# Optimization experiments

Measured on AMD Instinct MI355X. Metric: run time of the kernel, lower is better.

## Reference

```python
import jax, jax.numpy as jnp
import numpy as np

EPS = 1e-5  # BatchNorm3d default eps


def setup_inputs() -> dict:
    key = jax.random.key(0)
    ks = jax.random.split(key, 8)
    B, C, T, H, W = 2, 256, 8, 28, 28
    P, NS = 128, 5
    sc = 0.02  # keep activations stable through 5 residual stages
    return {
        "x": jax.random.normal(ks[0], (B, C, T, H, W), jnp.float32),
        "Wt": jax.random.normal(ks[1], (P, C), jnp.float32) * sc,
        "Wp": jax.random.normal(ks[2], (P, C), jnp.float32) * sc,
        "Wg": jax.random.normal(ks[3], (NS, P, C), jnp.float32) * sc,
        "W1": jax.random.normal(ks[4], (NS, C, P), jnp.float32) * sc,
        "W2": jax.random.normal(ks[5], (NS, C, P), jnp.float32) * sc,
        "gamma": jnp.ones((NS, C), jnp.float32),
        "beta": jnp.zeros((NS, C), jnp.float32),
    }


def _batchnorm(x, g, b):
    # x: [B, C, S]; training-mode BN over (batch, spatial) per channel
    mu = jnp.mean(x, axis=(0, 2), keepdims=True)
    var = jnp.var(x, axis=(0, 2), keepdims=True)
    xn = (x - mu) * jax.lax.rsqrt(var + EPS)
    return xn * g[None, :, None] + b[None, :, None]


def reference(x, Wt, Wp, Wg, W1, W2, gamma, beta):
    B, C, T, H, W = x.shape
    S = T * H * W
    xf = x.reshape(B, C, S)                      # [B,C,S]
    # DotKernel: att[b,i,j] = softmax_j( t[b,i,:] . p[b,:,j] )
    t = jnp.einsum("bcs,pc->bsp", xf, Wt)        # [B,S,P]
    p = jnp.einsum("bcs,pc->bps", xf, Wp)        # [B,P,S]
    att = jax.nn.softmax(jnp.einsum("bsp,bpq->bsq", t, p), axis=-1)  # [B,S,S]

    out = xf
    n_stages = Wg.shape[0]
    for i in range(n_stages):  # small fixed stage count
        g = jnp.einsum("bcs,pc->bsp", out, Wg[i])          # [B,S,P]
        x1 = jnp.einsum("bsp,cp->bcs", g, W1[i])           # w_1(g)
        x2 = jnp.einsum("bsq,bqp->bsp", att, g)            # att @ g
        x2 = jnp.einsum("bsp,cp->bcs", x2, W2[i])          # w_2(...)
        out = _batchnorm(x1 + x2, gamma[i], beta[i]) + out  # BN + residual
    return out.reshape(B, C, T, H, W)
```

## Files before the change

kernel.cpp:

```cpp
#include <hip/hip_runtime.h>

#define B_  2
#define C_  256
#define S_  6272
#define P_  128
#define NS_ 5
#define KS_ 7
#define KCH_ 896
#define EPS_ 1e-5f
#define TPAD 264

typedef __attribute__((ext_vector_type(8))) short short8;
typedef __attribute__((ext_vector_type(4))) float f32x4;

__device__ __forceinline__ ushort f2bf(float f) {
    union { float f; unsigned u; } v; v.f = f;
    unsigned r = v.u + 0x7fffu + ((v.u >> 16) & 1u);
    return (ushort)(r >> 16);
}
__device__ __forceinline__ float bf2f(ushort h) {
    union { unsigned u; float f; } v; v.u = ((unsigned)h) << 16;
    return v.f;
}

__device__ __forceinline__ void gload16(const ushort* g, ushort* lds) {
    __builtin_amdgcn_global_load_lds(
        (const __attribute__((address_space(1))) void*)g,
        (__attribute__((address_space(3))) void*)lds, 16, 0, 0);
}

__global__ void k_convert_weights(const float* __restrict__ Wt, const float* __restrict__ Wp,
                                  const float* __restrict__ Wg, const float* __restrict__ W1,
                                  const float* __restrict__ W2,
                                  ushort* __restrict__ Wtpb,
                                  ushort* __restrict__ Wgb, ushort* __restrict__ catb,
                                  float* __restrict__ statb) {
    int i = blockIdx.x * 256 + threadIdx.x;
    const int nWtp = 2 * P_ * C_;
    const int nWg  = NS_ * P_ * C_;
    const int nCat = NS_ * C_ * 2 * P_;
    if (i < nWtp) {
        int c = i & (C_ - 1), row = i >> 8;
        float v = (row < P_) ? Wt[row * C_ + c] : Wp[(row - P_) * C_ + c];
        Wtpb[i] = f2bf(v);
    }
    if (i < nWg) { Wgb[i] = f2bf(Wg[i]); }
    if (i < nCat) {
        int k  = i & 255;
        int c  = (i >> 8) & (C_ - 1);
        int st = i >> 16;
        float v = (k < P_) ? W1[((size_t)st * C_ + c) * P_ + k]
                           : W2[((size_t)st * C_ + c) * P_ + (k - P_)];
        catb[i] = f2bf(v);
    }
    if (i < NS_ * 2 * C_) statb[i] = 0.f;
}

__global__ __launch_bounds__(256)
void k_init_x(const float* __restrict__ x, float* __restrict__ out,
              ushort* __restrict__ xb_sc) {
    __shared__ ushort tl[64][TPAD];
    const int bs = blockIdx.x;
    const int b = bs / 98, s0 = (bs - b * 98) * 64;
    const int tid = threadIdx.x, sl = tid & 63, cg = tid >> 6;
    #pragma unroll 4
    for (int it = 0; it < 64; ++it) {
        int c = it * 4 + cg;
        long idx = ((long)b * C_ + c) * S_ + s0 + sl;
        float v = x[idx];
        out[idx] = v;
        tl[sl][c] = f2bf(v);
    }
    __syncthreads();
    ushort* xs = xb_sc + ((long)b * S_ + s0) * C_;
    #pragma unroll
    for (int u0 = 0; u0 < 2048; u0 += 256) {
        int u = u0 + tid;
        int s = u >> 5, c8 = (u & 31) << 3;
        short8 w = *(const short8*)&tl[s][c8];
        *(short8*)&xs[(long)s * C_ + c8] = w;
    }
}

template <int MODE>
__global__ __launch_bounds__(256, 2)
void k_gemm(const ushort* __restrict__ A, const ushort* __restrict__ Bm,
            void* __restrict__ Out, ushort* __restrict__ OutT, float* __restrict__ Stat,
            int M, int N, int K, int lda, int ldb, int ldo, int ldot,
            long sA, long sB, long sOb, long sOch, long sOT, int nks, int kch) {
    const int z = blockIdx.z;
    const int b = z / nks, ch = z - b * nks;
    A  += (long)b * sA;
    Bm += (long)b * sB;
    const int k0 = ch * kch;

    const int bm = blockIdx.x * 128, bn = blockIdx.y * 128;

    __shared__ ushort Al[2][128][32];
    __shared__ ushort Bl[2][128][32];

    const int tid = threadIdx.x, lane = tid & 63, wid = tid >> 6;
    const int wr = (wid >> 1) * 64, wc = (wid & 1) * 64;
    const int r16 = lane & 15, kg = lane >> 4;

    const int st_row = lane >> 2;
    const int st_slot = lane & 3;
    const int st_gk8 = ((st_slot ^ ((st_row >> 1) & 3)) << 3);
    const int sw8 = ((kg ^ ((r16 >> 1) & 3)) << 3);

    const ushort* Arow0 = A + (long)(bm + wid * 32 + st_row) * lda + st_gk8;
    const ushort* Arow1 = A + (long)(bm + wid * 32 + 16 + st_row) * lda + st_gk8;
    const ushort* Brow0 = Bm + (long)(bn + wid * 32 + st_row) * ldb + st_gk8;
    const ushort* Brow1 = Bm + (long)(bn + wid * 32 + 16 + st_row) * ldb + st_gk8;

    f32x4 acc[4][4];
    #pragma unroll
    for (int i = 0; i < 4; ++i)
        #pragma unroll
        for (int j = 0; j < 4; ++j)
            acc[i][j] = (f32x4){0.f, 0.f, 0.f, 0.f};

    auto stage = [&](int kk, int buf) {
        gload16(Arow0 + kk, &Al[buf][wid * 32][0]);
        gload16(Arow1 + kk, &Al[buf][wid * 32 + 16][0]);
        gload16(Brow0 + kk, &Bl[buf][wid * 32][0]);
        gload16(Brow1 + kk, &Bl[buf][wid * 32 + 16][0]);
    };
    auto compute = [&](int buf) {
        short8 af[4], bfv[4];
        #pragma unroll
        for (int i = 0; i < 4; ++i)
            af[i] = *(const short8*)&Al[buf][wr + i * 16 + r16][sw8];
        #pragma unroll
        for (int j = 0; j < 4; ++j)
            bfv[j] = *(const short8*)&Bl[buf][wc + j * 16 + r16][sw8];
        #pragma unroll
        for (int i = 0; i < 4; ++i)
            #pragma unroll
            for (int j = 0; j < 4; ++j)
                acc[i][j] = __builtin_amdgcn_mfma_f32_16x16x32_bf16(af[i], bfv[j], acc[i][j], 0, 0, 0);
    };

    const int nt = kch >> 5;
    stage(k0, 0);
    __syncthreads();
    int cur = 0;
    for (int t = 0; t < nt - 1; ++t) {
        stage(k0 + (t + 1) * 32, cur ^ 1);
        compute(cur);
        __syncthreads();
        cur ^= 1;
    }
    compute(cur);

    const int orow0 = bm + wr + kg * 4;
    const int ocol0 = bn + wc + r16;
    if (MODE == 2 || MODE == 3) {
        float* O = (float*)Out + (long)b * sOb + (long)ch * sOch;
        #pragma unroll
        for (int i = 0; i < 4; ++i)
            #pragma unroll
            for (int j = 0; j < 4; ++j)
                #pragma unroll
                for (int q = 0; q < 4; ++q)
                    O[(long)(orow0 + i * 16 + q) * ldo + (ocol0 + j * 16)] = acc[i][j][q];
        if (MODE == 3) {
            #pragma unroll
            for (int i = 0; i < 4; ++i)
                #pragma unroll
                for (int q = 0; q < 4; ++q) {
                    float s1 = acc[i][0][q] + acc[i][1][q] + acc[i][2][q] + acc[i][3][q];
                    float s2 = acc[i][0][q] * acc[i][0][q] + acc[i][1][q] * acc[i][1][q]
                             + acc[i][2][q] * acc[i][2][q] + acc[i][3][q] * acc[i][3][q];
                    #pragma unroll
                    for (int off = 1; off < 16; off <<= 1) {
                        s1 += __shfl_xor(s1, off);
                        s2 += __shfl_xor(s2, off);
                    }
                    if (r16 == 0) {
                        atomicAdd(&Stat[orow0 + i * 16 + q], s1);
                        atomicAdd(&Stat[M + orow0 + i * 16 + q], s2);
                    }
                }
        }
    } else {
        ushort* O = (ushort*)Out + (long)b * sOb + (long)ch * sOch;
        ushort* OT = (MODE == 1) ? (OutT + (long)b * sOT) : nullptr;
        #pragma unroll
        for (int i = 0; i < 4; ++i)
            #pragma unroll
            for (int j = 0; j < 4; ++j)
                #pragma unroll
                for (int q = 0; q < 4; ++q) {
                    ushort h = f2bf(acc[i][j][q]);
                    O[(long)(orow0 + i * 16 + q) * ldo + (ocol0 + j * 16)] = h;
                    if (MODE == 1)
                        OT[(long)(ocol0 + j * 16) * ldot + (orow0 + i * 16 + q)] = h;
                }
    }
}

__global__ __launch_bounds__(256)
void k_softmax(ushort* __restrict__ att) {
    long row = blockIdx.x;
    ushort* r = att + row * (long)S_;
    const int tid = threadIdx.x;
    __shared__ float red1[4];
    __shared__ float red2[4];
    const bool tail = tid < 16;

    short8 u0 = *(const short8*)&r[(0 * 256 + tid) * 8];
    short8 u1 = *(const short8*)&r[(1 * 256 + tid) * 8];
    short8 u2 = *(const short8*)&r[(2 * 256 + tid) * 8];
    short8 u3 = tail ? *(const short8*)&r[(768 + tid) * 8] : short8{0,0,0,0,0,0,0,0};

    float v[32];
    #pragma unroll
    for (int j = 0; j < 8; ++j) {
        v[j]      = bf2f((ushort)u0[j]);
        v[8 + j]  = bf2f((ushort)u1[j]);
        v[16 + j] = bf2f((ushort)u2[j]);
        v[24 + j] = tail ? bf2f((ushort)u3[j]) : -1e30f;
    }
    float mx = -1e30f;
    #pragma unroll
    for (int j = 0; j < 32; ++j) mx = fmaxf(mx, v[j]);
    #pragma unroll
    for (int off = 32; off; off >>= 1) mx = fmaxf(mx, __shfl_xor(mx, off));
    if ((tid & 63) == 0) red1[tid >> 6] = mx;
    __syncthreads();
    mx = fmaxf(fmaxf(red1[0], red1[1]), fmaxf(red1[2], red1[3]));

    float sum = 0.f;
    #pragma unroll
    for (int j = 0; j < 32; ++j) {
        float e = __expf(v[j] - mx);
        v[j] = e;
        sum += e;
    }
    #pragma unroll
    for (int off = 32; off; off >>= 1) sum += __shfl_xor(sum, off);
    if ((tid & 63) == 0) red2[tid >> 6] = sum;
    __syncthreads();
    sum = red2[0] + red2[1] + red2[2] + red2[3];
    float inv = 1.f / sum;

    short8 w0, w1, w2, w3;
    #pragma unroll
    for (int j = 0; j < 8; ++j) {
        w0[j] = (short)f2bf(v[j] * inv);
        w1[j] = (short)f2bf(v[8 + j] * inv);
        w2[j] = (short)f2bf(v[16 + j] * inv);
        w3[j] = (short)f2bf(v[24 + j] * inv);
    }
    *(short8*)&r[(0 * 256 + tid) * 8] = w0;
    *(short8*)&r[(1 * 256 + tid) * 8] = w1;
    *(short8*)&r[(2 * 256 + tid) * 8] = w2;
    if (tail) *(short8*)&r[(768 + tid) * 8] = w3;
}

__global__ void k_reduce_split(const float* __restrict__ split, ushort* __restrict__ BcatT) {
    long i = (long)blockIdx.x * 256 + threadIdx.x;
    if (i >= (long)B_ * S_ * P_) return;
    int p = (int)(i & (P_ - 1));
    long sp = i >> 7;
    int b = (int)(sp / S_);
    long s = sp - (long)b * S_;
    const float* base = split + (long)b * KS_ * S_ * P_ + s * P_ + p;
    float acc = 0.f;
    #pragma unroll
    for (int ch = 0; ch < KS_; ++ch) acc += base[(long)ch * S_ * P_];
    BcatT[((long)b * S_ + s) * 256 + 128 + p] = f2bf(acc);
}

__global__ __launch_bounds__(256)
void k_bn_apply(const float* __restrict__ y, const float* __restrict__ Stat,
                const float* __restrict__ gamma, const float* __restrict__ beta,
                float* __restrict__ out, ushort* __restrict__ xb_sc) {
    __shared__ ushort tl[64][TPAD];
    const int bs = blockIdx.x;
    const int b = bs / 98, s0 = (bs - b * 98) * 64;
    const int tid = threadIdx.x, sl = tid & 63, cg = tid >> 6;
    const float invn = 1.f / (float)(B_ * S_);
    #pragma unroll 4
    for (int it = 0; it < 64; ++it) {
        int c = it * 4 + cg;
        float m = Stat[c] * invn;
        float var = Stat[C_ + c] * invn - m * m;
        float rs = rsqrtf(var + EPS_);
        float sc = rs * gamma[c];
        float sh = beta[c] - m * sc;
        long idx = ((long)b * C_ + c) * S_ + s0 + sl;
        float v = out[idx] + y[idx] * sc + sh;
        out[idx] = v;
        tl[sl][c] = f2bf(v);
    }
    __syncthreads();
    ushort* xs = xb_sc + ((long)b * S_ + s0) * C_;
    #pragma unroll
    for (int u0 = 0; u0 < 2048; u0 += 256) {
        int u = u0 + tid;
        int s = u >> 5, c8 = (u & 31) << 3;
        short8 w = *(const short8*)&tl[s][c8];
        *(short8*)&xs[(long)s * C_ + c8] = w;
    }
}

extern "C" void kernel_launch(void* const* d_in, const int* in_sizes, int n_in,
                              void* d_out, int out_size, void* d_ws, size_t ws_size,
                              hipStream_t stream) {
    const float* x     = (const float*)d_in[0];
    const float* Wt    = (const float*)d_in[1];
    const float* Wp    = (const float*)d_in[2];
    const float* Wg    = (const float*)d_in[3];
    const float* W1    = (const float*)d_in[4];
    const float* W2    = (const float*)d_in[5];
    const float* gamma = (const float*)d_in[6];
    const float* beta  = (const float*)d_in[7];
    float* out = (float*)d_out;

    char* ws = (char*)d_ws;
    size_t off = 0;
    auto alloc = [&](size_t bytes) -> void* {
        void* p = ws + off;
        off = (off + bytes + 255) & ~(size_t)255;
        return p;
    };
    ushort* att   = (ushort*)alloc((size_t)B_ * S_ * S_ * 2);
    ushort* tpb   = (ushort*)alloc((size_t)B_ * S_ * 256 * 2);
    ushort* gTb   = (ushort*)alloc((size_t)B_ * P_ * S_ * 2);
    ushort* BcatT = (ushort*)alloc((size_t)B_ * S_ * 256 * 2);
    ushort* xbsc  = (ushort*)alloc((size_t)B_ * S_ * C_ * 2);
    float*  y     = (float*)alloc((size_t)B_ * C_ * S_ * 4);
    float*  split = (float*)alloc((size_t)B_ * KS_ * S_ * P_ * 4);
    ushort* Wtpb  = (ushort*)alloc((size_t)2 * P_ * C_ * 2);
    ushort* Wgb   = (ushort*)alloc((size_t)NS_ * P_ * C_ * 2);
    ushort* catb  = (ushort*)alloc((size_t)NS_ * C_ * 256 * 2);
    float*  statb = (float*)alloc((size_t)NS_ * 2 * C_ * 4);
    if (off > ws_size) return;

    dim3 blk(256);

    k_convert_weights<<<1280, 256, 0, stream>>>(Wt, Wp, Wg, W1, W2, Wtpb, Wgb, catb, statb);
    k_init_x<<<B_ * 98, 256, 0, stream>>>(x, out, xbsc);

    k_gemm<0><<<dim3(S_ / 128, 2, B_), blk, 0, stream>>>(
        xbsc, Wtpb, tpb, nullptr, nullptr, S_, 256, C_, C_, C_, 256, 0,
        (long)S_ * C_, 0, (long)S_ * 256, 0, 0, 1, C_);
    k_gemm<0><<<dim3(S_ / 128, S_ / 128, B_), blk, 0, stream>>>(
        tpb, tpb + 128, att, nullptr, nullptr, S_, S_, P_, 256, 256, S_, 0,
        (long)S_ * 256, (long)S_ * 256, (long)S_ * S_, 0, 0, 1, P_);
    k_softmax<<<B_ * S_, 256, 0, stream>>>(att);

    for (int i = 0; i < NS_; ++i) {
        k_gemm<1><<<dim3(S_ / 128, 1, B_), blk, 0, stream>>>(
            xbsc, Wgb + (size_t)i * P_ * C_, BcatT, gTb, nullptr,
            S_, P_, C_, C_, C_, 256, S_,
            (long)S_ * C_, 0, (long)S_ * 256, 0, (long)P_ * S_, 1, C_);
        k_gemm<2><<<dim3(S_ / 128, 1, B_ * KS_), blk, 0, stream>>>(
            att, gTb, split, nullptr, nullptr, S_, P_, S_, S_, S_, P_, 0,
            (long)S_ * S_, (long)P_ * S_, (long)KS_ * S_ * P_, (long)S_ * P_, 0, KS_, KCH_);
        k_reduce_split<<<(int)(((long)B_ * S_ * P_ + 255) / 256), 256, 0, stream>>>(split, BcatT);
        k_gemm<3><<<dim3(C_ / 128, S_ / 128, B_), blk, 0, stream>>>(
            catb + (size_t)i * C_ * 256, BcatT, y, nullptr, statb + (size_t)i * 2 * C_,
            C_, S_, 256, 256, 256, S_, 0,
            0, (long)S_ * 256, (long)C_ * S_, 0, 0, 1, 256);
        k_bn_apply<<<B_ * 98, 256, 0, stream>>>(y, statb + (size_t)i * 2 * C_,
                                                gamma + i * C_, beta + i * C_, out, xbsc);
    }
}
```

Measured before the change: 722.5 us.

## Stage bf16 GEMM epilogue through LDS and store split-K partials in bf16

```diff
diff --git a/kernel.cpp b/kernel.cpp
--- a/kernel.cpp
+++ b/kernel.cpp
@@ -98,6 +98,7 @@
 
     __shared__ ushort Al[2][128][32];
     __shared__ ushort Bl[2][128][32];
+    __shared__ ushort ep[32][130];
 
     const int tid = threadIdx.x, lane = tid & 63, wid = tid >> 6;
     const int wr = (wid >> 1) * 64, wc = (wid & 1) * 64;
@@ -155,7 +156,7 @@
 
     const int orow0 = bm + wr + kg * 4;
     const int ocol0 = bn + wc + r16;
-    if (MODE == 2 || MODE == 3) {
+    if (MODE == 3) {
         float* O = (float*)Out + (long)b * sOb + (long)ch * sOch;
         #pragma unroll
         for (int i = 0; i < 4; ++i)
@@ -164,39 +165,56 @@
                 #pragma unroll
                 for (int q = 0; q < 4; ++q)
                     O[(long)(orow0 + i * 16 + q) * ldo + (ocol0 + j * 16)] = acc[i][j][q];
-        if (MODE == 3) {
-            #pragma unroll
-            for (int i = 0; i < 4; ++i)
-                #pragma unroll
-                for (int q = 0; q < 4; ++q) {
-                    float s1 = acc[i][0][q] + acc[i][1][q] + acc[i][2][q] + acc[i][3][q];
-                    float s2 = acc[i][0][q] * acc[i][0][q] + acc[i][1][q] * acc[i][1][q]
-                             + acc[i][2][q] * acc[i][2][q] + acc[i][3][q] * acc[i][3][q];
-                    #pragma unroll
-                    for (int off = 1; off < 16; off <<= 1) {
-                        s1 += __shfl_xor(s1, off);
-                        s2 += __shfl_xor(s2, off);
-                    }
-                    if (r16 == 0) {
-                        atomicAdd(&Stat[orow0 + i * 16 + q], s1);
-                        atomicAdd(&Stat[M + orow0 + i * 16 + q], s2);
-                    }
+        #pragma unroll
+        for (int i = 0; i < 4; ++i)
+            #pragma unroll
+            for (int q = 0; q < 4; ++q) {
+                float s1 = acc[i][0][q] + acc[i][1][q] + acc[i][2][q] + acc[i][3][q];
+                float s2 = acc[i][0][q] * acc[i][0][q] + acc[i][1][q] * acc[i][1][q]
+                         + acc[i][2][q] * acc[i][2][q] + acc[i][3][q] * acc[i][3][q];
+                #pragma unroll
+                for (int off = 1; off < 16; off <<= 1) {
+                    s1 += __shfl_xor(s1, off);
+                    s2 += __shfl_xor(s2, off);
                 }
-        }
+                if (r16 == 0) {
+                    atomicAdd(&Stat[orow0 + i * 16 + q], s1);
+                    atomicAdd(&Stat[M + orow0 + i * 16 + q], s2);
+                }
+            }
     } else {
         ushort* O = (ushort*)Out + (long)b * sOb + (long)ch * sOch;
         ushort* OT = (MODE == 1) ? (OutT + (long)b * sOT) : nullptr;
-        #pragma unroll
-        for (int i = 0; i < 4; ++i)
+        const int wrH = wid >> 1;
+        #pragma unroll
+        for (int i = 0; i < 4; ++i) {
+            __syncthreads();
             #pragma unroll
             for (int j = 0; j < 4; ++j)
                 #pragma unroll
-                for (int q = 0; q < 4; ++q) {
-                    ushort h = f2bf(acc[i][j][q]);
-                    O[(long)(orow0 + i * 16 + q) * ldo + (ocol0 + j * 16)] = h;
-                    if (MODE == 1)
-                        OT[(long)(ocol0 + j * 16) * ldot + (orow0 + i * 16 + q)] = h;
-                }
+                for (int q = 0; q < 4; ++q)
+                    ep[wrH * 16 + kg * 4 + q][wc + j * 16 + r16] = f2bf(acc[i][j][q]);
+            __syncthreads();
+            #pragma unroll
+            for (int p = 0; p < 2; ++p) {
+                int r = p * 16 + (tid >> 4);
+                int c8 = (tid & 15) << 3;
+                short8 w = *(const short8*)&ep[r][c8];
+                int grow = bm + (r >> 4) * 64 + i * 16 + (r & 15);
+                *(short8*)&O[(long)grow * ldo + bn + c8] = w;
+            }
+            if (MODE == 1) {
+                int c = tid >> 1, h = tid & 1;
+                short8 w0, w1;
+                #pragma unroll
+                for (int r = 0; r < 8; ++r) w0[r] = (short)ep[h * 16 + r][c];
+                #pragma unroll
+                for (int r = 0; r < 8; ++r) w1[r] = (short)ep[h * 16 + 8 + r][c];
+                long obase = (long)(bn + c) * ldot + bm + h * 64 + i * 16;
+                *(short8*)&OT[obase] = w0;
+                *(short8*)&OT[obase + 8] = w1;
+            }
+        }
     }
 }
 
@@ -259,18 +277,25 @@
     if (tail) *(short8*)&r[(768 + tid) * 8] = w3;
 }
 
-__global__ void k_reduce_split(const float* __restrict__ split, ushort* __restrict__ BcatT) {
+__global__ void k_reduce_split(const ushort* __restrict__ splitb, ushort* __restrict__ BcatT) {
     long i = (long)blockIdx.x * 256 + threadIdx.x;
-    if (i >= (long)B_ * S_ * P_) return;
-    int p = (int)(i & (P_ - 1));
-    long sp = i >> 7;
+    if (i >= (long)B_ * S_ * (P_ / 8)) return;
+    int p8 = (int)(i & (P_ / 8 - 1));
+    long sp = i >> 4;
     int b = (int)(sp / S_);
     long s = sp - (long)b * S_;
-    const float* base = split + (long)b * KS_ * S_ * P_ + s * P_ + p;
-    float acc = 0.f;
-    #pragma unroll
-    for (int ch = 0; ch < KS_; ++ch) acc += base[(long)ch * S_ * P_];
-    BcatT[((long)b * S_ + s) * 256 + 128 + p] = f2bf(acc);
+    const ushort* base = splitb + ((long)b * KS_ * S_ + s) * P_ + p8 * 8;
+    float acc[8] = {0.f, 0.f, 0.f, 0.f, 0.f, 0.f, 0.f, 0.f};
+    #pragma unroll
+    for (int ch = 0; ch < KS_; ++ch) {
+        short8 u = *(const short8*)&base[(long)ch * S_ * P_];
+        #pragma unroll
+        for (int j = 0; j < 8; ++j) acc[j] += bf2f((ushort)u[j]);
+    }
+    short8 w;
+    #pragma unroll
+    for (int j = 0; j < 8; ++j) w[j] = (short)f2bf(acc[j]);
+    *(short8*)&BcatT[((long)b * S_ + s) * 256 + 128 + p8 * 8] = w;
 }
 
 __global__ __launch_bounds__(256)
@@ -326,17 +351,17 @@
         off = (off + bytes + 255) & ~(size_t)255;
         return p;
     };
-    ushort* att   = (ushort*)alloc((size_t)B_ * S_ * S_ * 2);
-    ushort* tpb   = (ushort*)alloc((size_t)B_ * S_ * 256 * 2);
-    ushort* gTb   = (ushort*)alloc((size_t)B_ * P_ * S_ * 2);
-    ushort* BcatT = (ushort*)alloc((size_t)B_ * S_ * 256 * 2);
-    ushort* xbsc  = (ushort*)alloc((size_t)B_ * S_ * C_ * 2);
-    float*  y     = (float*)alloc((size_t)B_ * C_ * S_ * 4);
-    float*  split = (float*)alloc((size_t)B_ * KS_ * S_ * P_ * 4);
-    ushort* Wtpb  = (ushort*)alloc((size_t)2 * P_ * C_ * 2);
-    ushort* Wgb   = (ushort*)alloc((size_t)NS_ * P_ * C_ * 2);
-    ushort* catb  = (ushort*)alloc((size_t)NS_ * C_ * 256 * 2);
-    float*  statb = (float*)alloc((size_t)NS_ * 2 * C_ * 4);
+    ushort* att    = (ushort*)alloc((size_t)B_ * S_ * S_ * 2);
+    ushort* tpb    = (ushort*)alloc((size_t)B_ * S_ * 256 * 2);
+    ushort* gTb    = (ushort*)alloc((size_t)B_ * P_ * S_ * 2);
+    ushort* BcatT  = (ushort*)alloc((size_t)B_ * S_ * 256 * 2);
+    ushort* xbsc   = (ushort*)alloc((size_t)B_ * S_ * C_ * 2);
+    float*  y      = (float*)alloc((size_t)B_ * C_ * S_ * 4);
+    ushort* splitb = (ushort*)alloc((size_t)B_ * KS_ * S_ * P_ * 2);
+    ushort* Wtpb   = (ushort*)alloc((size_t)2 * P_ * C_ * 2);
+    ushort* Wgb    = (ushort*)alloc((size_t)NS_ * P_ * C_ * 2);
+    ushort* catb   = (ushort*)alloc((size_t)NS_ * C_ * 256 * 2);
+    float*  statb  = (float*)alloc((size_t)NS_ * 2 * C_ * 4);
     if (off > ws_size) return;
 
     dim3 blk(256);
@@ -357,10 +382,10 @@
             xbsc, Wgb + (size_t)i * P_ * C_, BcatT, gTb, nullptr,
             S_, P_, C_, C_, C_, 256, S_,
             (long)S_ * C_, 0, (long)S_ * 256, 0, (long)P_ * S_, 1, C_);
-        k_gemm<2><<<dim3(S_ / 128, 1, B_ * KS_), blk, 0, stream>>>(
-            att, gTb, split, nullptr, nullptr, S_, P_, S_, S_, S_, P_, 0,
+        k_gemm<0><<<dim3(S_ / 128, 1, B_ * KS_), blk, 0, stream>>>(
+            att, gTb, splitb, nullptr, nullptr, S_, P_, S_, S_, S_, P_, 0,
             (long)S_ * S_, (long)P_ * S_, (long)KS_ * S_ * P_, (long)S_ * P_, 0, KS_, KCH_);
-        k_reduce_split<<<(int)(((long)B_ * S_ * P_ + 255) / 256), 256, 0, stream>>>(split, BcatT);
+        k_reduce_split<<<784, 256, 0, stream>>>(splitb, BcatT);
         k_gemm<3><<<dim3(C_ / 128, S_ / 128, B_), blk, 0, stream>>>(
             catb + (size_t)i * C_ * 256, BcatT, y, nullptr, statb + (size_t)i * 2 * C_,
             C_, S_, 256, 256, 256, S_, 0,
```

Result: faster. 699.2 us (-3.2%).
